# Optimization experiments

Measured on AMD Instinct MI355X. Metric: run time of the kernel, lower is better.

The kernel has to match this reference:

```python
import jax, jax.numpy as jnp
import numpy as np

N_NODES = 100000
N_EDGES = 640000
IN_DIM = 128
# PyG SAGEConv pyramid per SageCox(num_layers=4)
DIMS = [128, 85, 56, 28, 1]  # 85=int(128*2/3), 56=int(85*2/3), 28=int(56/2)


def setup_inputs() -> dict:
    key = jax.random.key(0)
    ks = jax.random.split(key, 2 + 3 * 4)
    inp = {
        "x": jax.random.normal(ks[0], (N_NODES, IN_DIM), dtype=jnp.float32),
        "edge_index": jax.random.randint(ks[1], (2, N_EDGES), 0, N_NODES, dtype=jnp.int64),
    }
    # Per-layer params: lin_l (weight+bias, applied to aggregated neighbors),
    # lin_r (weight only, applied to root features) -- PyG SAGEConv defaults.
    for i in range(4):
        din, dout = DIMS[i], DIMS[i + 1]
        inp[f"Wl{i}"] = jax.random.normal(ks[2 + 3 * i], (din, dout), dtype=jnp.float32) * 0.05
        inp[f"bl{i}"] = jax.random.normal(ks[3 + 3 * i], (dout,), dtype=jnp.float32) * 0.05
        inp[f"Wr{i}"] = jax.random.normal(ks[4 + 3 * i], (din, dout), dtype=jnp.float32) * 0.05
    return inp


def _sage_layer(x, src, dst, Wl, bl, Wr):
    # mean aggregation of source-node features at destination nodes
    msg = x[src]                                            # [E, din] gather
    agg = jax.ops.segment_sum(msg, dst, num_segments=N_NODES)
    deg = jax.ops.segment_sum(jnp.ones((src.shape[0],), x.dtype), dst,
                              num_segments=N_NODES)
    mean = agg / jnp.maximum(deg, 1.0)[:, None]             # [N, din]
    return mean @ Wl + bl + x @ Wr                          # [N, dout]


def reference(x, edge_index, Wl0, bl0, Wr0, Wl1, bl1, Wr1, Wl2, bl2, Wr2, Wl3, bl3, Wr3):
    src, dst = edge_index[0], edge_index[1]
    params = [(Wl0, bl0, Wr0), (Wl1, bl1, Wr1), (Wl2, bl2, Wr2), (Wl3, bl3, Wr3)]
    for Wl, bl, Wr in params:
        x = _sage_layer(x, src, dst, Wl, bl, Wr)
    return x  # [N, 1] risk scores
```

## Files before the change

### kernel.cpp

```cpp
#include <hip/hip_runtime.h>


#define NNODES 100000
#define NEDGES 640000

using bf16x8 = __attribute__((ext_vector_type(8))) short;
using f32x4  = __attribute__((ext_vector_type(4))) float;

__device__ __forceinline__ unsigned short f2bf(float f) {
    union { float f; unsigned u; } v; v.f = f;
    unsigned r = v.u + 0x7fffu + ((v.u >> 16) & 1u);
    return (unsigned short)(r >> 16);
}
__device__ __forceinline__ float bf2f(unsigned b) {
    union { unsigned u; float f; } v; v.u = b << 16;
    return v.f;
}


__global__ void hist_kernel(const int* __restrict__ edst, int* __restrict__ deg, int E) {
    int i = blockIdx.x * blockDim.x + threadIdx.x;
    if (i < E) atomicAdd(&deg[edst[i]], 1);
}

__global__ void scanA_kernel(const int* __restrict__ deg, int* __restrict__ bsum, int N) {
    __shared__ int s[256];
    int i = blockIdx.x * 256 + threadIdx.x;
    s[threadIdx.x] = (i < N) ? deg[i] : 0;
    __syncthreads();
    for (int off = 128; off > 0; off >>= 1) {
        if (threadIdx.x < off) s[threadIdx.x] += s[threadIdx.x + off];
        __syncthreads();
    }
    if (threadIdx.x == 0) bsum[blockIdx.x] = s[0];
}

__global__ void scanB_kernel(const int* __restrict__ bsum, int* __restrict__ bpre, int nb) {
    __shared__ int s[512];
    int t = threadIdx.x;
    int v = (t < nb) ? bsum[t] : 0;
    s[t] = v;
    __syncthreads();
    for (int off = 1; off < 512; off <<= 1) {
        int add = (t >= off) ? s[t - off] : 0;
        __syncthreads();
        s[t] += add;
        __syncthreads();
    }
    if (t < nb) bpre[t] = s[t] - v;
}

__global__ void scanC_kernel(const int* __restrict__ deg, const int* __restrict__ bpre,
                             int* __restrict__ rowptr, int* __restrict__ cursor, int N, int E) {
    __shared__ int s[256];
    int t = threadIdx.x;
    int i = blockIdx.x * 256 + t;
    int v = (i < N) ? deg[i] : 0;
    s[t] = v;
    __syncthreads();
    for (int off = 1; off < 256; off <<= 1) {
        int add = (t >= off) ? s[t - off] : 0;
        __syncthreads();
        s[t] += add;
        __syncthreads();
    }
    if (i < N) {
        int excl = bpre[blockIdx.x] + s[t] - v;
        rowptr[i] = excl;
        cursor[i] = excl;
        if (i == N - 1) rowptr[N] = E;
    }
}

__global__ void fill_kernel(const int* __restrict__ esrc, const int* __restrict__ edst,
                            int* __restrict__ cursor, int* __restrict__ csr, int E) {
    int i = blockIdx.x * blockDim.x + threadIdx.x;
    if (i < E) {
        int pos = atomicAdd(&cursor[edst[i]], 1);
        csr[pos] = esrc[i];
    }
}


__device__ __forceinline__ void packT_one(const float* Wl, const float* Wr,
                                          unsigned short* WcT, int idx, int DIN,
                                          int KP, int DOUT, int DOUTP) {
    int c = idx / KP, k = idx - c * KP;
    float v = 0.0f;
    if (k < DIN) {
        if (c < DOUT) v = Wl[k * DOUT + c];
        else if (c >= DOUTP && c < DOUTP + DOUT) v = Wr[k * DOUT + (c - DOUTP)];
    }
    WcT[idx] = f2bf(v);
}

__global__ void packAll_kernel(const float* __restrict__ Wl0, const float* __restrict__ Wr0,
                               const float* __restrict__ Wl1, const float* __restrict__ Wr1,
                               const float* __restrict__ Wl2, const float* __restrict__ Wr2,
                               unsigned short* __restrict__ Wc0,
                               unsigned short* __restrict__ Wc1,
                               unsigned short* __restrict__ Wc2) {
    const int S0 = 192 * 128, S1 = 128 * 96, S2 = 64 * 64;
    int idx = blockIdx.x * blockDim.x + threadIdx.x;
    if (idx < S0) packT_one(Wl0, Wr0, Wc0, idx, 128, 128, 85, 96);
    else if (idx < S0 + S1) packT_one(Wl1, Wr1, Wc1, idx - S0, 85, 96, 56, 64);
    else if (idx < S0 + S1 + S2) packT_one(Wl2, Wr2, Wc2, idx - S0 - S1, 56, 64, 28, 32);
}


template <bool XFP32, int KP, int SIN, int NTILES, int DOUT, int SPP>
__global__ void __launch_bounds__(256)
projm_kernel(const void* __restrict__ xin,
             const unsigned short* __restrict__ WcT,
             const float* __restrict__ bl,
             unsigned short* __restrict__ p,
             unsigned short* __restrict__ acc_out, int N) {
    constexpr int KT   = KP / 32;
    constexpr int HT   = NTILES / 2;
    constexpr int CW   = NTILES * 16;
    constexpr int WSTR = KP + 8;
    constexpr int LSTR = SPP + 8;
    static_assert(HT * 16 == SPP, "phase width must equal SPP");
    __shared__ short wS[CW * WSTR];
    __shared__ short oS[128 * LSTR];

    const int lane = threadIdx.x & 63;
    const int wave = threadIdx.x >> 6;
    const int l15 = lane & 15;
    const int lk  = lane >> 4;
    const int row0 = blockIdx.x * 128;
    const int wrow = wave * 32;

    for (int c8 = threadIdx.x; c8 < CW * (KP / 8); c8 += 256) {
        const int c  = c8 / (KP / 8);
        const int k8 = c8 - c * (KP / 8);
        *(bf16x8*)(wS + c * WSTR + k8 * 8) =
            *(const bf16x8*)(WcT + (size_t)c * KP + k8 * 8);
    }

    bf16x8 afrag[2][KT];
#pragma unroll
    for (int h = 0; h < 2; ++h) {
        int arow = row0 + wrow + h * 16 + l15;
        if (arow >= N) arow = N - 1;
        if constexpr (XFP32) {
            const float* xr = (const float*)xin + (size_t)arow * SIN + lk * 8;
#pragma unroll
            for (int kt = 0; kt < KT; ++kt) {
                const float4 a = *(const float4*)(xr + kt * 32);
                const float4 b = *(const float4*)(xr + kt * 32 + 4);
                bf16x8 v;
                v[0] = (short)f2bf(a.x); v[1] = (short)f2bf(a.y);
                v[2] = (short)f2bf(a.z); v[3] = (short)f2bf(a.w);
                v[4] = (short)f2bf(b.x); v[5] = (short)f2bf(b.y);
                v[6] = (short)f2bf(b.z); v[7] = (short)f2bf(b.w);
                afrag[h][kt] = v;
            }
        } else {
            const unsigned short* xr = (const unsigned short*)xin + (size_t)arow * SIN + lk * 8;
#pragma unroll
            for (int kt = 0; kt < KT; ++kt)
                afrag[h][kt] = *(const bf16x8*)(xr + kt * 32);
        }
    }

    __syncthreads();

    const int rows_here = min(128, N - row0);
    const int cnt8 = rows_here * (SPP / 8);

#pragma unroll
    for (int ph = 0; ph < 2; ++ph) {
#pragma unroll 2
        for (int nt = 0; nt < HT; ++nt) {
            const short* wp = wS + (size_t)((ph * HT + nt) * 16 + l15) * WSTR + lk * 8;
            bf16x8 bfrag[KT];
#pragma unroll
            for (int kt = 0; kt < KT; ++kt)
                bfrag[kt] = *(const bf16x8*)(wp + kt * 32);

            f32x4 a0 = {0.f, 0.f, 0.f, 0.f};
            f32x4 a1 = {0.f, 0.f, 0.f, 0.f};
#pragma unroll
            for (int kt = 0; kt < KT; ++kt) {
                a0 = __builtin_amdgcn_mfma_f32_16x16x32_bf16(afrag[0][kt], bfrag[kt], a0, 0, 0, 0);
                a1 = __builtin_amdgcn_mfma_f32_16x16x32_bf16(afrag[1][kt], bfrag[kt], a1, 0, 0, 0);
            }

            const int co = nt * 16 + l15;
            const float bias = (ph == 1 && co < DOUT) ? bl[co] : 0.0f;
#pragma unroll
            for (int h = 0; h < 2; ++h) {
                const f32x4 a = h ? a1 : a0;
                const int rl = wrow + h * 16 + lk * 4;
#pragma unroll
                for (int j = 0; j < 4; ++j)
                    oS[(rl + j) * LSTR + co] = (short)f2bf(a[j] + bias);
            }
        }

        __syncthreads();

        unsigned short* dst = ph ? acc_out : p;
        for (int e8 = threadIdx.x; e8 < cnt8; e8 += 256) {
            const int row = e8 / (SPP / 8);
            const int c8  = e8 - row * (SPP / 8);
            *(bf16x8*)(dst + (size_t)row0 * SPP + (size_t)e8 * 8) =
                *(const bf16x8*)(oS + row * LSTR + c8 * 8);
        }

        __syncthreads();
    }
}


template <int DOUT, int SP, int SN>
__global__ void __launch_bounds__(256)
gatherb_kernel(const int* __restrict__ rowptr, const int* __restrict__ csr,
               const unsigned short* __restrict__ p, const unsigned short* __restrict__ acc,
               unsigned short* __restrict__ xnext, int N) {
    const int node = __builtin_amdgcn_readfirstlane((blockIdx.x * 256 + threadIdx.x) >> 6);
    const int lane = threadIdx.x & 63;
    if (node >= N) return;
    const int beg = rowptr[node], end = rowptr[node + 1];
    const float inv = 1.0f / (float)max(end - beg, 1);
    constexpr int NPAIR = (DOUT + 1) / 2;
    const int co = 2 * lane;

    float s0 = 0.f, s1 = 0.f, s2 = 0.f, s3 = 0.f;
    float h0 = 0.f, h1 = 0.f, h2 = 0.f, h3 = 0.f;
    if (lane < NPAIR) {
        int j = beg;
        for (; j + 4 <= end; j += 4) {
            const unsigned u0 = *(const unsigned*)(p + (size_t)csr[j]     * SP + co);
            const unsigned u1 = *(const unsigned*)(p + (size_t)csr[j + 1] * SP + co);
            const unsigned u2 = *(const unsigned*)(p + (size_t)csr[j + 2] * SP + co);
            const unsigned u3 = *(const unsigned*)(p + (size_t)csr[j + 3] * SP + co);
            s0 += bf2f(u0 & 0xffffu); h0 += bf2f(u0 >> 16);
            s1 += bf2f(u1 & 0xffffu); h1 += bf2f(u1 >> 16);
            s2 += bf2f(u2 & 0xffffu); h2 += bf2f(u2 >> 16);
            s3 += bf2f(u3 & 0xffffu); h3 += bf2f(u3 >> 16);
        }
        for (; j < end; ++j) {
            const unsigned u0 = *(const unsigned*)(p + (size_t)csr[j] * SP + co);
            s0 += bf2f(u0 & 0xffffu); h0 += bf2f(u0 >> 16);
        }
    }
    if (co < SN) {
        const float slo = (s0 + s1) + (s2 + s3);
        const float shi = (h0 + h1) + (h2 + h3);
        float lo = 0.f, hi = 0.f;
        if (co < DOUT)     lo = bf2f((unsigned)acc[(size_t)node * SP + co])     + inv * slo;
        if (co + 1 < DOUT) hi = bf2f((unsigned)acc[(size_t)node * SP + co + 1]) + inv * shi;
        const unsigned w = (unsigned)f2bf(lo) | ((unsigned)f2bf(hi) << 16);
        *(unsigned*)(xnext + (size_t)node * SN + co) = w;
    }
}


__global__ void __launch_bounds__(256)
gather2g_kernel(const int* __restrict__ rowptr, const int* __restrict__ csr,
                const unsigned short* __restrict__ p, const unsigned short* __restrict__ acc,
                const float* __restrict__ Wl3, const float* __restrict__ bl3,
                const float* __restrict__ Wr3,
                float* __restrict__ p3, float* __restrict__ out, int N) {
    const int node = __builtin_amdgcn_readfirstlane((blockIdx.x * 256 + threadIdx.x) >> 6);
    const int lane = threadIdx.x & 63;
    if (node >= N) return;
    const int beg = rowptr[node], end = rowptr[node + 1];
    const float inv = 1.0f / (float)max(end - beg, 1);
    const int co = 2 * lane;

    float s0 = 0.f, s1 = 0.f, s2 = 0.f, s3 = 0.f;
    float h0 = 0.f, h1 = 0.f, h2 = 0.f, h3 = 0.f;
    if (lane < 14) {
        int j = beg;
        for (; j + 4 <= end; j += 4) {
            const unsigned u0 = *(const unsigned*)(p + (size_t)csr[j]     * 32 + co);
            const unsigned u1 = *(const unsigned*)(p + (size_t)csr[j + 1] * 32 + co);
            const unsigned u2 = *(const unsigned*)(p + (size_t)csr[j + 2] * 32 + co);
            const unsigned u3 = *(const unsigned*)(p + (size_t)csr[j + 3] * 32 + co);
            s0 += bf2f(u0 & 0xffffu); h0 += bf2f(u0 >> 16);
            s1 += bf2f(u1 & 0xffffu); h1 += bf2f(u1 >> 16);
            s2 += bf2f(u2 & 0xffffu); h2 += bf2f(u2 >> 16);
            s3 += bf2f(u3 & 0xffffu); h3 += bf2f(u3 >> 16);
        }
        for (; j < end; ++j) {
            const unsigned u0 = *(const unsigned*)(p + (size_t)csr[j] * 32 + co);
            s0 += bf2f(u0 & 0xffffu); h0 += bf2f(u0 >> 16);
        }
    }
    float xlo = 0.f, xhi = 0.f, wl0 = 0.f, wl1 = 0.f, wr0 = 0.f, wr1 = 0.f;
    if (lane < 14) {
        xlo = bf2f((unsigned)acc[(size_t)node * 32 + co])     + inv * ((s0 + s1) + (s2 + s3));
        xhi = bf2f((unsigned)acc[(size_t)node * 32 + co + 1]) + inv * ((h0 + h1) + (h2 + h3));
        wl0 = Wl3[co]; wl1 = Wl3[co + 1];
        wr0 = Wr3[co]; wr1 = Wr3[co + 1];
    }
    float sl = xlo * wl0 + xhi * wl1;
    float sr = xlo * wr0 + xhi * wr1;
#pragma unroll
    for (int off = 32; off > 0; off >>= 1) {
        sl += __shfl_xor(sl, off, 64);
        sr += __shfl_xor(sr, off, 64);
    }
    if (lane == 0) {
        p3[node] = sl;
        out[node] = sr + bl3[0];
    }
}

__global__ void gather1_kernel(const int* __restrict__ rowptr, const int* __restrict__ csr,
                               const float* __restrict__ p, float* __restrict__ out, int N) {
    const int node = blockIdx.x * blockDim.x + threadIdx.x;
    if (node >= N) return;
    const int beg = rowptr[node], end = rowptr[node + 1];
    const float inv = 1.0f / (float)max(end - beg, 1);
    float a0 = 0.f, a1 = 0.f, a2 = 0.f, a3 = 0.f;
    int j = beg;
    for (; j + 4 <= end; j += 4) {
        a0 += p[csr[j]]; a1 += p[csr[j + 1]]; a2 += p[csr[j + 2]]; a3 += p[csr[j + 3]];
    }
    for (; j < end; ++j) a0 += p[csr[j]];
    out[node] += inv * ((a0 + a1) + (a2 + a3));
}


extern "C" void kernel_launch(void* const* d_in, const int* in_sizes, int n_in,
                              void* d_out, int out_size, void* d_ws, size_t ws_size,
                              hipStream_t stream) {
    const float* x  = (const float*)d_in[0];
    const int*   ei = (const int*)d_in[1];
    const int N = NNODES;
    const int E = NEDGES;
    const int* esrc = ei;
    const int* edst = ei + E;

    const float* Wl[4] = {(const float*)d_in[2], (const float*)d_in[5],
                          (const float*)d_in[8], (const float*)d_in[11]};
    const float* bl[4] = {(const float*)d_in[3], (const float*)d_in[6],
                          (const float*)d_in[9], (const float*)d_in[12]};
    const float* Wr[4] = {(const float*)d_in[4], (const float*)d_in[7],
                          (const float*)d_in[10], (const float*)d_in[13]};

    char* base = (char*)d_ws;
    size_t off = 0;
    auto alloc = [&](size_t bytes) {
        char* r = base + off;
        off += (bytes + 255) & ~(size_t)255;
        return r;
    };
    unsigned short* pB   = (unsigned short*)alloc((size_t)N * 96 * 2);
    unsigned short* accB = (unsigned short*)alloc((size_t)N * 96 * 2);
    unsigned short* xp   = (unsigned short*)alloc((size_t)N * 96 * 2);
    float*          p3   = (float*)alloc((size_t)N * 4);
    unsigned short* Wc0  = (unsigned short*)alloc((size_t)192 * 128 * 2);
    unsigned short* Wc1  = (unsigned short*)alloc((size_t)128 * 96 * 2);
    unsigned short* Wc2  = (unsigned short*)alloc((size_t)64 * 64 * 2);
    int* degi   = (int*)alloc((size_t)N * 4);
    int* rowptr = (int*)alloc((size_t)(N + 1) * 4);
    int* cursor = (int*)alloc((size_t)N * 4);
    int* csr    = (int*)alloc((size_t)E * 4);
    int* bsum   = (int*)alloc(512 * 4);
    int* bpre   = (int*)alloc(512 * 4);

    unsigned short* x2 = xp;

    const int nb = (N + 255) / 256;

    hipMemsetAsync(degi, 0, (size_t)N * sizeof(int), stream);
    hist_kernel<<<(E + 255) / 256, 256, 0, stream>>>(edst, degi, E);
    scanA_kernel<<<nb, 256, 0, stream>>>(degi, bsum, N);
    scanB_kernel<<<1, 512, 0, stream>>>(bsum, bpre, nb);
    scanC_kernel<<<nb, 256, 0, stream>>>(degi, bpre, rowptr, cursor, N, E);
    fill_kernel<<<(E + 255) / 256, 256, 0, stream>>>(esrc, edst, cursor, csr, E);

    const int packTot = 192 * 128 + 128 * 96 + 64 * 64;
    packAll_kernel<<<(packTot + 255) / 256, 256, 0, stream>>>(
        Wl[0], Wr[0], Wl[1], Wr[1], Wl[2], Wr[2], Wc0, Wc1, Wc2);

    const int projBlocks = (N + 127) / 128;

    projm_kernel<true, 128, 128, 12, 85, 96><<<projBlocks, 256, 0, stream>>>(
        x, Wc0, bl[0], pB, accB, N);
    gatherb_kernel<85, 96, 96><<<(N + 3) / 4, 256, 0, stream>>>(
        rowptr, csr, pB, accB, xp, N);

    projm_kernel<false, 96, 96, 8, 56, 64><<<projBlocks, 256, 0, stream>>>(
        xp, Wc1, bl[1], pB, accB, N);
    gatherb_kernel<56, 64, 64><<<(N + 3) / 4, 256, 0, stream>>>(
        rowptr, csr, pB, accB, x2, N);

    projm_kernel<false, 64, 64, 4, 28, 32><<<projBlocks, 256, 0, stream>>>(
        x2, Wc2, bl[2], pB, accB, N);

    gather2g_kernel<<<(N + 3) / 4, 256, 0, stream>>>(
        rowptr, csr, pB, accB, Wl[3], bl[3], Wr[3], p3, (float*)d_out, N);
    gather1_kernel<<<(N + 255) / 256, 256, 0, stream>>>(
        rowptr, csr, p3, (float*)d_out, N);
}
```

Measured before the change: 254.9 us.

## Pack two nodes per wave in narrow gathers and halve projection weight LDS

After: 233.9 us. 8.2% less time.

```diff
diff --git a/kernel.cpp b/kernel.cpp
--- a/kernel.cpp
+++ b/kernel.cpp
@@ -117,11 +117,10 @@
              unsigned short* __restrict__ acc_out, int N) {
     constexpr int KT   = KP / 32;
     constexpr int HT   = NTILES / 2;
-    constexpr int CW   = NTILES * 16;
     constexpr int WSTR = KP + 8;
     constexpr int LSTR = SPP + 8;
     static_assert(HT * 16 == SPP, "phase width must equal SPP");
-    __shared__ short wS[CW * WSTR];
+    __shared__ short wS[HT * 16 * WSTR];
     __shared__ short oS[128 * LSTR];
 
     const int lane = threadIdx.x & 63;
@@ -131,12 +130,16 @@
     const int row0 = blockIdx.x * 128;
     const int wrow = wave * 32;
 
-    for (int c8 = threadIdx.x; c8 < CW * (KP / 8); c8 += 256) {
-        const int c  = c8 / (KP / 8);
-        const int k8 = c8 - c * (KP / 8);
-        *(bf16x8*)(wS + c * WSTR + k8 * 8) =
-            *(const bf16x8*)(WcT + (size_t)c * KP + k8 * 8);
-    }
+    auto stageW = [&](int colbase) {
+        for (int c8 = threadIdx.x; c8 < HT * 16 * (KP / 8); c8 += 256) {
+            const int c  = c8 / (KP / 8);
+            const int k8 = c8 - c * (KP / 8);
+            *(bf16x8*)(wS + c * WSTR + k8 * 8) =
+                *(const bf16x8*)(WcT + (size_t)(colbase + c) * KP + k8 * 8);
+        }
+    };
+
+    stageW(0);
 
     bf16x8 afrag[2][KT];
 #pragma unroll
@@ -169,11 +172,10 @@
     const int rows_here = min(128, N - row0);
     const int cnt8 = rows_here * (SPP / 8);
 
-#pragma unroll
-    for (int ph = 0; ph < 2; ++ph) {
+    auto computePhase = [&](bool withBias) {
 #pragma unroll 2
         for (int nt = 0; nt < HT; ++nt) {
-            const short* wp = wS + (size_t)((ph * HT + nt) * 16 + l15) * WSTR + lk * 8;
+            const short* wp = wS + (size_t)(nt * 16 + l15) * WSTR + lk * 8;
             bf16x8 bfrag[KT];
 #pragma unroll
             for (int kt = 0; kt < KT; ++kt)
@@ -188,7 +190,7 @@
             }
 
             const int co = nt * 16 + l15;
-            const float bias = (ph == 1 && co < DOUT) ? bl[co] : 0.0f;
+            const float bias = (withBias && co < DOUT) ? bl[co] : 0.0f;
 #pragma unroll
             for (int h = 0; h < 2; ++h) {
                 const f32x4 a = h ? a1 : a0;
@@ -198,38 +200,52 @@
                     oS[(rl + j) * LSTR + co] = (short)f2bf(a[j] + bias);
             }
         }
-
-        __syncthreads();
-
-        unsigned short* dst = ph ? acc_out : p;
+    };
+
+    auto storeOut = [&](unsigned short* dst) {
         for (int e8 = threadIdx.x; e8 < cnt8; e8 += 256) {
             const int row = e8 / (SPP / 8);
             const int c8  = e8 - row * (SPP / 8);
             *(bf16x8*)(dst + (size_t)row0 * SPP + (size_t)e8 * 8) =
                 *(const bf16x8*)(oS + row * LSTR + c8 * 8);
         }
-
-        __syncthreads();
-    }
-}
-
-
-template <int DOUT, int SP, int SN>
+    };
+
+    computePhase(false);
+    __syncthreads();
+    storeOut(p);
+    stageW(HT * 16);
+    __syncthreads();
+    computePhase(true);
+    __syncthreads();
+    storeOut(acc_out);
+}
+
+
+template <int DOUT, int SP, int SN, int NPW>
 __global__ void __launch_bounds__(256)
 gatherb_kernel(const int* __restrict__ rowptr, const int* __restrict__ csr,
                const unsigned short* __restrict__ p, const unsigned short* __restrict__ acc,
                unsigned short* __restrict__ xnext, int N) {
-    const int node = __builtin_amdgcn_readfirstlane((blockIdx.x * 256 + threadIdx.x) >> 6);
+    const int wid  = (blockIdx.x * 256 + threadIdx.x) >> 6;
     const int lane = threadIdx.x & 63;
+    int node, hl;
+    if constexpr (NPW == 1) {
+        node = __builtin_amdgcn_readfirstlane(wid);
+        hl = lane;
+    } else {
+        node = wid * 2 + (lane >> 5);
+        hl = lane & 31;
+    }
     if (node >= N) return;
     const int beg = rowptr[node], end = rowptr[node + 1];
     const float inv = 1.0f / (float)max(end - beg, 1);
     constexpr int NPAIR = (DOUT + 1) / 2;
-    const int co = 2 * lane;
+    const int co = 2 * hl;
 
     float s0 = 0.f, s1 = 0.f, s2 = 0.f, s3 = 0.f;
     float h0 = 0.f, h1 = 0.f, h2 = 0.f, h3 = 0.f;
-    if (lane < NPAIR) {
+    if (hl < NPAIR) {
         int j = beg;
         for (; j + 4 <= end; j += 4) {
             const unsigned u0 = *(const unsigned*)(p + (size_t)csr[j]     * SP + co);
@@ -264,16 +280,18 @@
                 const float* __restrict__ Wl3, const float* __restrict__ bl3,
                 const float* __restrict__ Wr3,
                 float* __restrict__ p3, float* __restrict__ out, int N) {
-    const int node = __builtin_amdgcn_readfirstlane((blockIdx.x * 256 + threadIdx.x) >> 6);
+    const int wid  = (blockIdx.x * 256 + threadIdx.x) >> 6;
     const int lane = threadIdx.x & 63;
+    const int node = wid * 2 + (lane >> 5);
+    const int hl   = lane & 31;
     if (node >= N) return;
     const int beg = rowptr[node], end = rowptr[node + 1];
     const float inv = 1.0f / (float)max(end - beg, 1);
-    const int co = 2 * lane;
+    const int co = 2 * hl;
 
     float s0 = 0.f, s1 = 0.f, s2 = 0.f, s3 = 0.f;
     float h0 = 0.f, h1 = 0.f, h2 = 0.f, h3 = 0.f;
-    if (lane < 14) {
+    if (hl < 14) {
         int j = beg;
         for (; j + 4 <= end; j += 4) {
             const unsigned u0 = *(const unsigned*)(p + (size_t)csr[j]     * 32 + co);
@@ -291,7 +309,7 @@
         }
     }
     float xlo = 0.f, xhi = 0.f, wl0 = 0.f, wl1 = 0.f, wr0 = 0.f, wr1 = 0.f;
-    if (lane < 14) {
+    if (hl < 14) {
         xlo = bf2f((unsigned)acc[(size_t)node * 32 + co])     + inv * ((s0 + s1) + (s2 + s3));
         xhi = bf2f((unsigned)acc[(size_t)node * 32 + co + 1]) + inv * ((h0 + h1) + (h2 + h3));
         wl0 = Wl3[co]; wl1 = Wl3[co + 1];
@@ -300,11 +318,11 @@
     float sl = xlo * wl0 + xhi * wl1;
     float sr = xlo * wr0 + xhi * wr1;
 #pragma unroll
-    for (int off = 32; off > 0; off >>= 1) {
+    for (int off = 16; off > 0; off >>= 1) {
         sl += __shfl_xor(sl, off, 64);
         sr += __shfl_xor(sr, off, 64);
     }
-    if (lane == 0) {
+    if (hl == 0) {
         p3[node] = sl;
         out[node] = sr + bl3[0];
     }
@@ -383,18 +401,18 @@
 
     projm_kernel<true, 128, 128, 12, 85, 96><<<projBlocks, 256, 0, stream>>>(
         x, Wc0, bl[0], pB, accB, N);
-    gatherb_kernel<85, 96, 96><<<(N + 3) / 4, 256, 0, stream>>>(
+    gatherb_kernel<85, 96, 96, 1><<<(N + 3) / 4, 256, 0, stream>>>(
         rowptr, csr, pB, accB, xp, N);
 
     projm_kernel<false, 96, 96, 8, 56, 64><<<projBlocks, 256, 0, stream>>>(
         xp, Wc1, bl[1], pB, accB, N);
-    gatherb_kernel<56, 64, 64><<<(N + 3) / 4, 256, 0, stream>>>(
+    gatherb_kernel<56, 64, 64, 2><<<(N + 7) / 8, 256, 0, stream>>>(
         rowptr, csr, pB, accB, x2, N);
 
     projm_kernel<false, 64, 64, 4, 28, 32><<<projBlocks, 256, 0, stream>>>(
         x2, Wc2, bl[2], pB, accB, N);
 
-    gather2g_kernel<<<(N + 3) / 4, 256, 0, stream>>>(
+    gather2g_kernel<<<(N + 7) / 8, 256, 0, stream>>>(
         rowptr, csr, pB, accB, Wl[3], bl[3], Wr[3], p3, (float*)d_out, N);
     gather1_kernel<<<(N + 255) / 256, 256, 0, stream>>>(
         rowptr, csr, p3, (float*)d_out, N);
```
